# Kernel optimization log

Hardware: AMD Instinct MI355X
Metric: run time of the kernel (lower is better)

Reference implementation:

```python
import jax, jax.numpy as jnp
import numpy as np


def setup_inputs() -> dict:
    key = jax.random.key(0)
    k1, k2 = jax.random.split(key)
    video_feat = jax.random.normal(k1, (64, 2048, 512), dtype=jnp.float32)
    lang_feat = jax.random.normal(k2, (64, 512, 512), dtype=jnp.float32)
    return {"video_feat": video_feat, "lang_feat": lang_feat}


def reference(video_feat, lang_feat):
    # video_feat: [B, Nv, D], lang_feat: [B, Nl, D]
    a = jnp.sum(video_feat ** 2, axis=2, keepdims=True)          # [B, Nv, 1]
    b = jnp.sum(lang_feat ** 2, axis=2, keepdims=True)           # [B, Nl, 1]
    ab = jnp.einsum('bvd,bld->bvl', video_feat, lang_feat)       # [B, Nv, Nl]
    pairwise = a - 2.0 * ab + jnp.swapaxes(b, 1, 2)              # [B, Nv, Nl]
    Nv = pairwise.shape[1]
    Nl = pairwise.shape[2]
    lang_to_clip = jnp.sum(jnp.min(pairwise, axis=2), axis=1) / Nv  # [B]
    clip_to_lang = jnp.sum(jnp.min(pairwise, axis=1), axis=1) / Nl  # [B]
    return lang_to_clip + clip_to_lang
```

## Files before the change

### kernel.cpp

```cpp
#include <hip/hip_runtime.h>
#include <hip/hip_bf16.h>
#include <stdint.h>

#define NB 64
#define NV 2048
#define NL 512
#define DK 512
#define BT 128
#define BK 64

typedef __attribute__((ext_vector_type(8))) short bf16x8;
typedef __attribute__((ext_vector_type(4))) float f32x4;

__device__ __forceinline__ unsigned enc_f(float f) {
  unsigned u = __float_as_uint(f);
  return (u & 0x80000000u) ? ~u : (u | 0x80000000u);
}
__device__ __forceinline__ float dec_f(unsigned u) {
  unsigned b = (u & 0x80000000u) ? (u ^ 0x80000000u) : ~u;
  return __uint_as_float(b);
}

__device__ __forceinline__ unsigned short f2bf(float f) {
  unsigned u = __float_as_uint(f);
  u += 0x7FFFu + ((u >> 16) & 1u);
  return (unsigned short)(u >> 16);
}
__device__ __forceinline__ unsigned pack_bf2(float lo, float hi) {
  return (unsigned)f2bf(lo) | ((unsigned)f2bf(hi) << 16);
}

__device__ __forceinline__ void gload_lds16(const void* g, void* l) {
  __builtin_amdgcn_global_load_lds(
      (const __attribute__((address_space(1))) unsigned*)g,
      (__attribute__((address_space(3))) unsigned*)l, 16, 0, 0);
}

__global__ __launch_bounds__(256) void convert_norm(
    const float* __restrict__ video, const float* __restrict__ lang,
    unsigned short* __restrict__ Vb, unsigned short* __restrict__ Lb,
    float* __restrict__ vnorm, float* __restrict__ lnorm,
    unsigned* __restrict__ rowmin, unsigned* __restrict__ colmin) {
  const int t = threadIdx.x;
  const int lane = t & 63;
  const int row = blockIdx.x * 4 + (t >> 6);
  const int rows_v = NB * NV;

  const float* src;
  unsigned short* dst;
  float* nrm;
  unsigned* sent;
  size_t r;
  if (row < rows_v) { src = video; dst = Vb; nrm = vnorm; sent = rowmin; r = (size_t)row; }
  else              { src = lang;  dst = Lb;  nrm = lnorm; sent = colmin; r = (size_t)(row - rows_v); }

  const float4* p = (const float4*)(src + r * DK);
  const float4 a = p[lane * 2];
  const float4 b = p[lane * 2 + 1];

  float n = a.x * a.x + a.y * a.y + a.z * a.z + a.w * a.w
          + b.x * b.x + b.y * b.y + b.z * b.z + b.w * b.w;
  #pragma unroll
  for (int m = 1; m < 64; m <<= 1) n += __shfl_xor(n, m, 64);

  uint4 pk;
  pk.x = pack_bf2(a.x, a.y); pk.y = pack_bf2(a.z, a.w);
  pk.z = pack_bf2(b.x, b.y); pk.w = pack_bf2(b.z, b.w);
  ((uint4*)(dst + r * DK))[lane] = pk;
  if (lane == 0) {
    nrm[r] = n;
    sent[r] = 0xFFFFFFFFu;
  }
}

__global__ __launch_bounds__(256, 4) void chamfer_gemm(
    const unsigned short* __restrict__ Vb, const unsigned short* __restrict__ Lb,
    const float* __restrict__ vnorm, const float* __restrict__ lnorm,
    unsigned* __restrict__ rowmin, unsigned* __restrict__ colmin) {
  __shared__ unsigned short Asm[BT][BK];
  __shared__ unsigned short Bsm[BT][BK];

  const int bid0 = blockIdx.x;
  const int bid = (bid0 & 7) * 512 + (bid0 >> 3);
  const int b  = bid >> 6;
  const int vt = (bid >> 2) & 15;
  const int lt = bid & 3;

  const unsigned short* Ag = Vb + ((size_t)b * NV + (size_t)vt * BT) * DK;
  const unsigned short* Bg = Lb + ((size_t)b * NL + (size_t)lt * BT) * DK;

  const int t = threadIdx.x;
  const int lane = t & 63;
  const int w = t >> 6;
  const int wrow = (w >> 1) * 64;
  const int wcol = (w & 1) * 64;

  const int lr = lane >> 3;
  const int lp = lane & 7;
  const int schunk = lp ^ lr;

  f32x4 acc[4][4];
  #pragma unroll
  for (int i = 0; i < 4; i++)
    #pragma unroll
    for (int j = 0; j < 4; j++)
      acc[i][j] = (f32x4){0.f, 0.f, 0.f, 0.f};

  const int c16 = lane & 15;
  const int hi  = lane >> 4;
  const int sw  = c16 & 7;

  for (int k0 = 0; k0 < DK; k0 += BK) {
    __syncthreads();
    #pragma unroll
    for (int s = 0; s < 4; s++) {
      const int row = w * 32 + s * 8 + lr;
      gload_lds16(Ag + (size_t)row * DK + k0 + schunk * 8, &Asm[w * 32 + s * 8][0]);
      gload_lds16(Bg + (size_t)row * DK + k0 + schunk * 8, &Bsm[w * 32 + s * 8][0]);
    }
    __syncthreads();
    #pragma unroll
    for (int ks = 0; ks < 2; ks++) {
      const int ck = ks * 4 + hi;
      bf16x8 af[4], bfr[4];
      #pragma unroll
      for (int i = 0; i < 4; i++)
        af[i] = *(const bf16x8*)&Asm[wrow + i * 16 + c16][(ck ^ sw) * 8];
      #pragma unroll
      for (int j = 0; j < 4; j++)
        bfr[j] = *(const bf16x8*)&Bsm[wcol + j * 16 + c16][(ck ^ sw) * 8];
      #pragma unroll
      for (int i = 0; i < 4; i++)
        #pragma unroll
        for (int j = 0; j < 4; j++)
          acc[i][j] = __builtin_amdgcn_mfma_f32_16x16x32_bf16(af[i], bfr[j], acc[i][j], 0, 0, 0);
    }
  }

  const int g = hi;
  const int c = c16;
  const size_t rowbase = (size_t)b * NV + (size_t)vt * BT + wrow;
  const size_t colbase = (size_t)b * NL + (size_t)lt * BT + wcol;

  float cn[4];
  #pragma unroll
  for (int j = 0; j < 4; j++) cn[j] = lnorm[colbase + j * 16 + c];

  float cmin[4];
  #pragma unroll
  for (int j = 0; j < 4; j++) cmin[j] = 3.0e38f;

  #pragma unroll
  for (int i = 0; i < 4; i++) {
    #pragma unroll
    for (int r = 0; r < 4; r++) {
      const float rn = vnorm[rowbase + i * 16 + g * 4 + r];
      float m = 3.0e38f;
      #pragma unroll
      for (int j = 0; j < 4; j++) {
        const float P = rn + cn[j] - 2.0f * acc[i][j][r];
        m = fminf(m, P);
        cmin[j] = fminf(cmin[j], P);
      }
      #pragma unroll
      for (int mm = 1; mm < 16; mm <<= 1)
        m = fminf(m, __shfl_xor(m, mm, 64));
      if (c == 0)
        atomicMin(&rowmin[rowbase + i * 16 + g * 4 + r], enc_f(m));
    }
  }
  #pragma unroll
  for (int j = 0; j < 4; j++) {
    float m = cmin[j];
    m = fminf(m, __shfl_xor(m, 16, 64));
    m = fminf(m, __shfl_xor(m, 32, 64));
    if (g == 0)
      atomicMin(&colmin[colbase + j * 16 + c], enc_f(m));
  }
}

__global__ void chamfer_reduce(const unsigned* __restrict__ rowmin,
                               const unsigned* __restrict__ colmin,
                               float* __restrict__ out) {
  const int b = blockIdx.x;
  const int t = threadIdx.x;
  float s = 0.f;
  for (int i = t; i < NV; i += 256) s += dec_f(rowmin[(size_t)b * NV + i]) * (1.0f / NV);
  for (int i = t; i < NL; i += 256) s += dec_f(colmin[(size_t)b * NL + i]) * (1.0f / NL);
  #pragma unroll
  for (int m = 1; m < 64; m <<= 1) s += __shfl_xor(s, m, 64);
  __shared__ float ws[4];
  if ((t & 63) == 0) ws[t >> 6] = s;
  __syncthreads();
  if (t == 0) out[b] = ws[0] + ws[1] + ws[2] + ws[3];
}

extern "C" void kernel_launch(void* const* d_in, const int* in_sizes, int n_in,
                              void* d_out, int out_size, void* d_ws, size_t ws_size,
                              hipStream_t stream) {
  const float* video = (const float*)d_in[0];
  const float* lang  = (const float*)d_in[1];
  float* out = (float*)d_out;

  const size_t vb_elems = (size_t)NB * NV * DK;
  const size_t lb_elems = (size_t)NB * NL * DK;

  unsigned short* Vb = (unsigned short*)d_ws;
  unsigned short* Lb = Vb + vb_elems;
  float* vnorm = (float*)(Lb + lb_elems);
  float* lnorm = vnorm + (size_t)NB * NV;
  unsigned* rowmin = (unsigned*)(lnorm + (size_t)NB * NL);
  unsigned* colmin = rowmin + (size_t)NB * NV;

  convert_norm<<<dim3((NB * NV + NB * NL) / 4), dim3(256), 0, stream>>>(
      video, lang, Vb, Lb, vnorm, lnorm, rowmin, colmin);
  chamfer_gemm<<<dim3(NB * 16 * 4), dim3(256), 0, stream>>>(
      Vb, Lb, vnorm, lnorm, rowmin, colmin);
  chamfer_reduce<<<dim3(NB), dim3(256), 0, stream>>>(rowmin, colmin, out);
}
```

Baseline: 523.1 us.

## Use 256x256 tiles with double-buffered LDS pipelining in chamfer GEMM

```diff
diff --git a/kernel.cpp b/kernel.cpp
--- a/kernel.cpp
+++ b/kernel.cpp
@@ -6,8 +6,10 @@
 #define NV 2048
 #define NL 512
 #define DK 512
-#define BT 128
+#define BM 256
+#define BN 256
 #define BK 64
+#define NT (DK / BK)
 
 typedef __attribute__((ext_vector_type(8))) short bf16x8;
 typedef __attribute__((ext_vector_type(4))) float f32x4;
@@ -73,91 +75,155 @@
   }
 }
 
-__global__ __launch_bounds__(256, 4) void chamfer_gemm(
+
+template <int C>
+__device__ __forceinline__ void ktile(
+    int t, int w, int wm, int wn, int c16, int hi,
+    const unsigned short* As, const unsigned short* Bs,
+    unsigned short (*Asm)[2][BM][32], unsigned short (*Bsm)[2][BN][32],
+    f32x4 (&acc)[8][4]) {
+  constexpr int N_ = C ^ 1;
+  const int tn = (t < NT - 1) ? t + 1 : t;
+  const int ko = tn * BK;
+
+  asm volatile("s_waitcnt vmcnt(4)" ::: "memory");
+  __builtin_amdgcn_s_barrier();
+
+  bf16x8 bf[4], af[4];
+  gload_lds16(As + ko,           &Asm[N_][0][w * 32][0]);
+  gload_lds16(As + 16 * DK + ko, &Asm[N_][0][w * 32 + 16][0]);
+  #pragma unroll
+  for (int j = 0; j < 4; ++j)
+    bf[j] = *(const bf16x8*)&Bsm[C][0][wn * 64 + j * 16 + c16][hi * 8];
+  #pragma unroll
+  for (int i = 0; i < 4; ++i)
+    af[i] = *(const bf16x8*)&Asm[C][0][wm * 128 + i * 16 + c16][hi * 8];
+  __builtin_amdgcn_s_setprio(1);
+  #pragma unroll
+  for (int i = 0; i < 4; ++i)
+    #pragma unroll
+    for (int j = 0; j < 4; ++j)
+      acc[i][j] = __builtin_amdgcn_mfma_f32_16x16x32_bf16(af[i], bf[j], acc[i][j], 0, 0, 0);
+  __builtin_amdgcn_s_setprio(0);
+
+  gload_lds16(Bs + ko,           &Bsm[N_][0][w * 32][0]);
+  gload_lds16(Bs + 16 * DK + ko, &Bsm[N_][0][w * 32 + 16][0]);
+  #pragma unroll
+  for (int i = 0; i < 4; ++i)
+    af[i] = *(const bf16x8*)&Asm[C][0][wm * 128 + 64 + i * 16 + c16][hi * 8];
+  __builtin_amdgcn_s_setprio(1);
+  #pragma unroll
+  for (int i = 0; i < 4; ++i)
+    #pragma unroll
+    for (int j = 0; j < 4; ++j)
+      acc[i + 4][j] = __builtin_amdgcn_mfma_f32_16x16x32_bf16(af[i], bf[j], acc[i + 4][j], 0, 0, 0);
+  __builtin_amdgcn_s_setprio(0);
+
+  asm volatile("s_waitcnt vmcnt(4)" ::: "memory");
+  __builtin_amdgcn_s_barrier();
+
+  gload_lds16(As + ko + 32,           &Asm[N_][1][w * 32][0]);
+  gload_lds16(As + 16 * DK + ko + 32, &Asm[N_][1][w * 32 + 16][0]);
+  #pragma unroll
+  for (int j = 0; j < 4; ++j)
+    bf[j] = *(const bf16x8*)&Bsm[C][1][wn * 64 + j * 16 + c16][hi * 8];
+  #pragma unroll
+  for (int i = 0; i < 4; ++i)
+    af[i] = *(const bf16x8*)&Asm[C][1][wm * 128 + i * 16 + c16][hi * 8];
+  __builtin_amdgcn_s_setprio(1);
+  #pragma unroll
+  for (int i = 0; i < 4; ++i)
+    #pragma unroll
+    for (int j = 0; j < 4; ++j)
+      acc[i][j] = __builtin_amdgcn_mfma_f32_16x16x32_bf16(af[i], bf[j], acc[i][j], 0, 0, 0);
+  __builtin_amdgcn_s_setprio(0);
+
+  gload_lds16(Bs + ko + 32,           &Bsm[N_][1][w * 32][0]);
+  gload_lds16(Bs + 16 * DK + ko + 32, &Bsm[N_][1][w * 32 + 16][0]);
+  #pragma unroll
+  for (int i = 0; i < 4; ++i)
+    af[i] = *(const bf16x8*)&Asm[C][1][wm * 128 + 64 + i * 16 + c16][hi * 8];
+  __builtin_amdgcn_s_setprio(1);
+  #pragma unroll
+  for (int i = 0; i < 4; ++i)
+    #pragma unroll
+    for (int j = 0; j < 4; ++j)
+      acc[i + 4][j] = __builtin_amdgcn_mfma_f32_16x16x32_bf16(af[i], bf[j], acc[i + 4][j], 0, 0, 0);
+  __builtin_amdgcn_s_setprio(0);
+}
+
+__global__ __launch_bounds__(512, 2) void chamfer_gemm(
     const unsigned short* __restrict__ Vb, const unsigned short* __restrict__ Lb,
     const float* __restrict__ vnorm, const float* __restrict__ lnorm,
     unsigned* __restrict__ rowmin, unsigned* __restrict__ colmin) {
-  __shared__ unsigned short Asm[BT][BK];
-  __shared__ unsigned short Bsm[BT][BK];
+  __shared__ unsigned short Asm[2][2][BM][32];
+  __shared__ unsigned short Bsm[2][2][BN][32];
 
   const int bid0 = blockIdx.x;
-  const int bid = (bid0 & 7) * 512 + (bid0 >> 3);
-  const int b  = bid >> 6;
-  const int vt = (bid >> 2) & 15;
-  const int lt = bid & 3;
-
-  const unsigned short* Ag = Vb + ((size_t)b * NV + (size_t)vt * BT) * DK;
-  const unsigned short* Bg = Lb + ((size_t)b * NL + (size_t)lt * BT) * DK;
+  const int bid = (bid0 & 7) * 128 + (bid0 >> 3);
+  const int b  = bid >> 4;
+  const int vt = (bid >> 1) & 7;
+  const int lt = bid & 1;
+
+  const unsigned short* Ag = Vb + ((size_t)b * NV + (size_t)vt * BM) * DK;
+  const unsigned short* Bg = Lb + ((size_t)b * NL + (size_t)lt * BN) * DK;
 
   const int t = threadIdx.x;
   const int lane = t & 63;
   const int w = t >> 6;
-  const int wrow = (w >> 1) * 64;
-  const int wcol = (w & 1) * 64;
-
-  const int lr = lane >> 3;
-  const int lp = lane & 7;
-  const int schunk = lp ^ lr;
-
-  f32x4 acc[4][4];
-  #pragma unroll
-  for (int i = 0; i < 4; i++)
-    #pragma unroll
-    for (int j = 0; j < 4; j++)
-      acc[i][j] = (f32x4){0.f, 0.f, 0.f, 0.f};
-
+  const int wm = w >> 2;
+  const int wn = w & 3;
   const int c16 = lane & 15;
   const int hi  = lane >> 4;
-  const int sw  = c16 & 7;
-
-  for (int k0 = 0; k0 < DK; k0 += BK) {
-    __syncthreads();
-    #pragma unroll
-    for (int s = 0; s < 4; s++) {
-      const int row = w * 32 + s * 8 + lr;
-      gload_lds16(Ag + (size_t)row * DK + k0 + schunk * 8, &Asm[w * 32 + s * 8][0]);
-      gload_lds16(Bg + (size_t)row * DK + k0 + schunk * 8, &Bsm[w * 32 + s * 8][0]);
-    }
-    __syncthreads();
-    #pragma unroll
-    for (int ks = 0; ks < 2; ks++) {
-      const int ck = ks * 4 + hi;
-      bf16x8 af[4], bfr[4];
-      #pragma unroll
-      for (int i = 0; i < 4; i++)
-        af[i] = *(const bf16x8*)&Asm[wrow + i * 16 + c16][(ck ^ sw) * 8];
-      #pragma unroll
-      for (int j = 0; j < 4; j++)
-        bfr[j] = *(const bf16x8*)&Bsm[wcol + j * 16 + c16][(ck ^ sw) * 8];
-      #pragma unroll
-      for (int i = 0; i < 4; i++)
-        #pragma unroll
-        for (int j = 0; j < 4; j++)
-          acc[i][j] = __builtin_amdgcn_mfma_f32_16x16x32_bf16(af[i], bfr[j], acc[i][j], 0, 0, 0);
-    }
-  }
-
-  const int g = hi;
-  const int c = c16;
-  const size_t rowbase = (size_t)b * NV + (size_t)vt * BT + wrow;
-  const size_t colbase = (size_t)b * NL + (size_t)lt * BT + wcol;
+
+  const int srow = w * 32 + (lane >> 2);
+  const unsigned short* As = Ag + (size_t)srow * DK + (lane & 3) * 8;
+  const unsigned short* Bs = Bg + (size_t)srow * DK + (lane & 3) * 8;
+
+  f32x4 acc[8][4];
+  #pragma unroll
+  for (int i = 0; i < 8; ++i)
+    #pragma unroll
+    for (int j = 0; j < 4; ++j)
+      acc[i][j] = (f32x4){0.f, 0.f, 0.f, 0.f};
+
+  gload_lds16(As,                &Asm[0][0][w * 32][0]);
+  gload_lds16(As + 16 * DK,      &Asm[0][0][w * 32 + 16][0]);
+  gload_lds16(Bs,                &Bsm[0][0][w * 32][0]);
+  gload_lds16(Bs + 16 * DK,      &Bsm[0][0][w * 32 + 16][0]);
+  gload_lds16(As + 32,           &Asm[0][1][w * 32][0]);
+  gload_lds16(As + 16 * DK + 32, &Asm[0][1][w * 32 + 16][0]);
+  gload_lds16(Bs + 32,           &Bsm[0][1][w * 32][0]);
+  gload_lds16(Bs + 16 * DK + 32, &Bsm[0][1][w * 32 + 16][0]);
+
+  #pragma unroll
+  for (int t2 = 0; t2 < NT; t2 += 2) {
+    ktile<0>(t2,     w, wm, wn, c16, hi, As, Bs, Asm, Bsm, acc);
+    ktile<1>(t2 + 1, w, wm, wn, c16, hi, As, Bs, Asm, Bsm, acc);
+  }
+
+  asm volatile("s_waitcnt vmcnt(0)" ::: "memory");
+  __builtin_amdgcn_s_barrier();
+
+  const size_t rowbase = (size_t)b * NV + (size_t)vt * BM + (size_t)wm * 128;
+  const size_t colbase = (size_t)b * NL + (size_t)lt * BN + (size_t)wn * 64;
 
   float cn[4];
   #pragma unroll
-  for (int j = 0; j < 4; j++) cn[j] = lnorm[colbase + j * 16 + c];
+  for (int j = 0; j < 4; ++j) cn[j] = lnorm[colbase + j * 16 + c16];
 
   float cmin[4];
   #pragma unroll
-  for (int j = 0; j < 4; j++) cmin[j] = 3.0e38f;
-
-  #pragma unroll
-  for (int i = 0; i < 4; i++) {
-    #pragma unroll
-    for (int r = 0; r < 4; r++) {
-      const float rn = vnorm[rowbase + i * 16 + g * 4 + r];
+  for (int j = 0; j < 4; ++j) cmin[j] = 3.0e38f;
+
+  #pragma unroll
+  for (int i = 0; i < 8; ++i) {
+    #pragma unroll
+    for (int r = 0; r < 4; ++r) {
+      const float rn = vnorm[rowbase + i * 16 + hi * 4 + r];
       float m = 3.0e38f;
       #pragma unroll
-      for (int j = 0; j < 4; j++) {
+      for (int j = 0; j < 4; ++j) {
         const float P = rn + cn[j] - 2.0f * acc[i][j][r];
         m = fminf(m, P);
         cmin[j] = fminf(cmin[j], P);
@@ -165,17 +231,17 @@
       #pragma unroll
       for (int mm = 1; mm < 16; mm <<= 1)
         m = fminf(m, __shfl_xor(m, mm, 64));
-      if (c == 0)
-        atomicMin(&rowmin[rowbase + i * 16 + g * 4 + r], enc_f(m));
+      if (c16 == 0)
+        atomicMin(&rowmin[rowbase + i * 16 + hi * 4 + r], enc_f(m));
     }
   }
   #pragma unroll
-  for (int j = 0; j < 4; j++) {
+  for (int j = 0; j < 4; ++j) {
     float m = cmin[j];
     m = fminf(m, __shfl_xor(m, 16, 64));
     m = fminf(m, __shfl_xor(m, 32, 64));
-    if (g == 0)
-      atomicMin(&colmin[colbase + j * 16 + c], enc_f(m));
+    if (hi == 0)
+      atomicMin(&colmin[colbase + j * 16 + c16], enc_f(m));
   }
 }
 
@@ -214,7 +280,7 @@
 
   convert_norm<<<dim3((NB * NV + NB * NL) / 4), dim3(256), 0, stream>>>(
       video, lang, Vb, Lb, vnorm, lnorm, rowmin, colmin);
-  chamfer_gemm<<<dim3(NB * 16 * 4), dim3(256), 0, stream>>>(
+  chamfer_gemm<<<dim3(NB * 16), dim3(512), 0, stream>>>(
       Vb, Lb, vnorm, lnorm, rowmin, colmin);
   chamfer_reduce<<<dim3(NB), dim3(256), 0, stream>>>(rowmin, colmin, out);
 }
```

Result: slower. 547.0 us (+4.6%).
